# Kernel optimization log

Measured on AMD Instinct MI355X. Metric: run time of the kernel, lower is better.

Reference implementation:

```python
import jax, jax.numpy as jnp
import numpy as np

T, H, DIN, N, E = 2048, 128, 17, 50000, 600000
SMILES_D, KMER_D = 574, 64


def _lstm_bidir(x, w_ih, w_hh, b_ih, b_hh):
    """Bidirectional LSTM layer. x: [T, Din]; weights stacked over direction: [2, 4H, *].
    Torch gate order: i, f, g, o."""
    Hh = w_hh.shape[-1]
    def run(d, reverse):
        xg = x @ w_ih[d].T + b_ih[d] + b_hh[d]  # [T, 4H] precomputed input gates
        def step(carry, xg_t):
            h, c = carry
            g = xg_t + h @ w_hh[d].T
            i, f, gg, o = jnp.split(g, 4)
            c = jax.nn.sigmoid(f) * c + jax.nn.sigmoid(i) * jnp.tanh(gg)
            h = jax.nn.sigmoid(o) * jnp.tanh(c)
            return (h, c), h
        init = (jnp.zeros((Hh,), x.dtype), jnp.zeros((Hh,), x.dtype))
        _, hs = jax.lax.scan(step, init, xg, reverse=reverse)
        return hs
    return jnp.concatenate([run(0, False), run(1, True)], axis=-1)  # [T, 2H]


def _forward(g_mol, feat_seq, smiles, kmer, edge_weight,
             w_ih0, w_hh0, b_ih0, b_hh0, w_ih1, w_hh1, b_ih1, b_hh1,
             Wq, bq, Wk, bk, Wv, bv, Wfc, bfc,
             W_gc1, b_gc1, W_gc2, b_gc2,
             W1, b1, W2, b2, W3, b3, W4, b4,
             edge_src, edge_dst):
    # ---- BiLSTM (2 layers, bidirectional, batch=1) + self-attention ----
    h = _lstm_bidir(g_mol, w_ih0, w_hh0, b_ih0, b_hh0)
    h = _lstm_bidir(h, w_ih1, w_hh1, b_ih1, b_hh1)            # [T, 2H]
    q = h @ Wq.T + bq
    k = h @ Wk.T + bk
    v = h @ Wv.T + bv                                          # [T, H]
    scores = (q @ k.T) / jnp.asarray(H ** 0.5, h.dtype)        # [T, T]
    attn_w = jax.nn.softmax(scores, axis=-1)
    gmol = (attn_w @ v)[-1] @ Wfc.T + bfc                      # [256] (last time step)
    ew = edge_weight[:, None]
    agg1 = jax.ops.segment_sum(feat_seq[edge_src] * ew, edge_dst, num_segments=N)
    h1 = jax.nn.relu(agg1 @ W_gc1 + b_gc1)                     # [N, 128]
    agg2 = jax.ops.segment_sum(h1[edge_src] * ew, edge_dst, num_segments=N)
    h2 = agg2 @ W_gc2 + b_gc2                                  # [N, 256]
    hg = jnp.mean(h2, axis=0)                                  # [256]
    # ---- MLP head ----
    feats = jnp.concatenate([hg, gmol, smiles, kmer])[None, :]  # [1, 1150]
    out = jax.nn.relu(feats @ W1.T + b1)
    out = jax.nn.relu(out @ W2.T + b2)
    out = jax.nn.relu(out @ W3.T + b3)
    out = out @ W4.T + b4                                       # [1, 1]
    return out, attn_w[None]                                    # attn weights [1, T, T]


def setup_inputs() -> dict:
    key = jax.random.key(0)
    ks = jax.random.split(key, 36)
    s = jnp.float32(0.05)
    def rn(k, shape):
        return jax.random.normal(k, shape, jnp.float32) * s
    return {
        "g_mol": jax.random.normal(ks[0], (T, DIN), jnp.float32),
        "feat_seq": jax.random.normal(ks[1], (N, H), jnp.float32),
        "smiles": jax.random.normal(ks[2], (SMILES_D,), jnp.float32),
        "kmer": jax.random.normal(ks[3], (KMER_D,), jnp.float32),
        "edge_weight": jax.random.uniform(ks[4], (E,), jnp.float32),
        "w_ih0": rn(ks[5], (2, 4 * H, DIN)),
        "w_hh0": rn(ks[6], (2, 4 * H, H)),
        "b_ih0": rn(ks[7], (2, 4 * H)),
        "b_hh0": rn(ks[8], (2, 4 * H)),
        "w_ih1": rn(ks[9], (2, 4 * H, 2 * H)),
        "w_hh1": rn(ks[10], (2, 4 * H, H)),
        "b_ih1": rn(ks[11], (2, 4 * H)),
        "b_hh1": rn(ks[12], (2, 4 * H)),
        "Wq": rn(ks[13], (H, 2 * H)), "bq": rn(ks[14], (H,)),
        "Wk": rn(ks[15], (H, 2 * H)), "bk": rn(ks[16], (H,)),
        "Wv": rn(ks[17], (H, 2 * H)), "bv": rn(ks[18], (H,)),
        "Wfc": rn(ks[19], (256, H)), "bfc": rn(ks[20], (256,)),
        "W_gc1": rn(ks[21], (H, H)), "b_gc1": rn(ks[22], (H,)),
        "W_gc2": rn(ks[23], (H, 256)), "b_gc2": rn(ks[24], (256,)),
        "W1": rn(ks[25], (575, 1150)), "b1": rn(ks[26], (575,)),
        "W2": rn(ks[27], (256, 575)), "b2": rn(ks[28], (256,)),
        "W3": rn(ks[29], (64, 256)), "b3": rn(ks[30], (64,)),
        "W4": rn(ks[31], (1, 64)), "b4": rn(ks[32], (1,)),
        "edge_src": jax.random.randint(ks[33], (E,), 0, N),
        "edge_dst": jax.random.randint(ks[34], (E,), 0, N),
    }


def reference(g_mol, feat_seq, smiles, kmer, edge_weight,
              w_ih0, w_hh0, b_ih0, b_hh0, w_ih1, w_hh1, b_ih1, b_hh1,
              Wq, bq, Wk, bk, Wv, bv, Wfc, bfc,
              W_gc1, b_gc1, W_gc2, b_gc2,
              W1, b1, W2, b2, W3, b3, W4, b4,
              edge_src, edge_dst):
    return _forward(g_mol, feat_seq, smiles, kmer, edge_weight,
                    w_ih0, w_hh0, b_ih0, b_hh0, w_ih1, w_hh1, b_ih1, b_hh1,
                    Wq, bq, Wk, bk, Wv, bv, Wfc, bfc,
                    W_gc1, b_gc1, W_gc2, b_gc2,
                    W1, b1, W2, b2, W3, b3, W4, b4,
                    edge_src, edge_dst)
```

## Files before the change

### kernel.cpp

```cpp
#include <hip/hip_runtime.h>
#include <stdint.h>


#define T_SEQ 2048
#define NNODE 50000
#define NEDGE 600000

typedef _Float16 half2_t __attribute__((ext_vector_type(2)));

static __device__ __forceinline__ float fast_rcp(float x) {
#if __has_builtin(__builtin_amdgcn_rcpf)
    return __builtin_amdgcn_rcpf(x);
#else
    return 1.f / x;
#endif
}
static __device__ __forceinline__ float exp2_fast(float x) {
#if __has_builtin(__builtin_amdgcn_exp2f)
    return __builtin_amdgcn_exp2f(x);
#else
    return exp2f(x);
#endif
}

static __device__ __forceinline__ float dot2h(float acc, uint32_t a, uint32_t b) {
#if __has_builtin(__builtin_amdgcn_fdot2)
    return __builtin_amdgcn_fdot2(__builtin_bit_cast(half2_t, a),
                                  __builtin_bit_cast(half2_t, b), acc, false);
#else
    half2_t ha = __builtin_bit_cast(half2_t, a);
    half2_t hb = __builtin_bit_cast(half2_t, b);
    return acc + (float)ha.x * (float)hb.x + (float)ha.y * (float)hb.y;
#endif
}

template<int CTRL>
static __device__ __forceinline__ float qperm(float x) {
    int r = __builtin_amdgcn_update_dpp(0, __builtin_bit_cast(int, x), CTRL, 0xF, 0xF, false);
    return __builtin_bit_cast(float, r);
}
#define QP_XOR1 0xB1
#define QP_XOR2 0x4E
#define QP_XOR3 0x1B

#define SIG_SCALE  (-1.44269504f)
#define TANH_SCALE ( 2.88539008f)

constexpr size_t OFF_XGT   = 0;
constexpr size_t OFF_HT0   = OFF_XGT + 2097152;
constexpr size_t OFF_HT1   = OFF_HT0 + 524288;
constexpr size_t OFF_Q     = OFF_HT1 + 524288;
constexpr size_t OFF_K     = OFF_Q + 262144;
constexpr size_t OFF_V     = OFF_K + 262144;
constexpr size_t OFF_AROW  = OFF_V + 262144;
constexpr size_t OFF_AV    = OFF_AROW + 2048;
constexpr size_t OFF_FEATS = OFF_AV + 128;
constexpr size_t OFF_F1    = OFF_FEATS + 1152;
constexpr size_t OFF_F2    = OFF_F1 + 576;
constexpr size_t OFF_GSUM  = OFF_F2 + 256;
constexpr size_t OFF_OUTW  = OFF_GSUM + 128;
constexpr size_t OFF_DEG   = OFF_OUTW + 50000;
constexpr size_t OFF_ROWP  = OFF_DEG + 50000;
constexpr size_t OFF_CUR   = OFF_ROWP + 50000;
constexpr size_t OFF_WPK   = OFF_CUR + 50000;
constexpr size_t OFF_EPACK = OFF_WPK + 131072;
constexpr size_t WS_WORDS  = OFF_EPACK + 1200000;

__global__ __launch_bounds__(256) void prep_kernel(
    const float* __restrict__ w_hh0, const float* __restrict__ w_hh1,
    uint32_t* __restrict__ wpk)
{
    int i = blockIdx.x * 256 + threadIdx.x;
    if (i >= 131072) return;
    int layer = i >> 16;
    int r = i & 65535;
    int kk = r & 15, m = (r >> 4) & 3, sidx = (r >> 6) & 3, q = (r >> 8) & 127, dirv = (r >> 15) & 1;
    const float* w = layer ? w_hh1 : w_hh0;
    const float* row = w + ((size_t)dirv * 512 + m * 128 + q) * 128;
    int k0 = 32 * sidx + 2 * kk;
    float sc = (m == 2) ? TANH_SCALE : SIG_SCALE;
    half2_t hv;
    hv.x = (_Float16)(row[k0] * sc);
    hv.y = (_Float16)(row[k0 + 1] * sc);
    wpk[i] = __builtin_bit_cast(uint32_t, hv);
}

__global__ __launch_bounds__(512) void xg0_kernel(
    const float* __restrict__ g_mol, const float* __restrict__ w_ih,
    const float* __restrict__ b_ih, const float* __restrict__ b_hh,
    float* __restrict__ xgT)
{
    int b = blockIdx.x;
    int dir = b >> 7, t0 = (b & 127) * 16;
    int r = threadIdx.x;
    __shared__ float xs[272];
    if (r < 272) xs[r] = g_mol[t0 * 17 + r];
    __syncthreads();
    const float* wrow = w_ih + (size_t)(dir * 512 + r) * 17;
    float wv[17];
#pragma unroll
    for (int k = 0; k < 17; ++k) wv[k] = wrow[k];
    float bias = b_ih[dir * 512 + r] + b_hh[dir * 512 + r];
    float rs = ((r >> 7) == 2) ? TANH_SCALE : SIG_SCALE;
    float acc[16];
#pragma unroll
    for (int tt = 0; tt < 16; ++tt) {
        float a = bias;
#pragma unroll
        for (int k = 0; k < 17; ++k) a += xs[tt * 17 + k] * wv[k];
        acc[tt] = a * rs;
    }
    float* orow = xgT + (size_t)(dir * 512 + r) * 2048 + t0;
    *(float4*)(orow + 0)  = make_float4(acc[0], acc[1], acc[2], acc[3]);
    *(float4*)(orow + 4)  = make_float4(acc[4], acc[5], acc[6], acc[7]);
    *(float4*)(orow + 8)  = make_float4(acc[8], acc[9], acc[10], acc[11]);
    *(float4*)(orow + 12) = make_float4(acc[12], acc[13], acc[14], acc[15]);
}

__global__ __launch_bounds__(512) void xg1_kernel(
    const float* __restrict__ hT0, const float* __restrict__ w_ih,
    const float* __restrict__ b_ih, const float* __restrict__ b_hh,
    float* __restrict__ xgT)
{
    int b = blockIdx.x;
    int dir = b >> 7, t0 = (b & 127) * 16;
    int tid = threadIdx.x;
    __shared__ float xs[16 * 256];
    for (int u = tid; u < 1024; u += 512) {
        int k = u >> 2, j4 = u & 3;
        float4 v = *(const float4*)(hT0 + (size_t)k * 2048 + t0 + 4 * j4);
        xs[(4 * j4 + 0) * 256 + k] = v.x;
        xs[(4 * j4 + 1) * 256 + k] = v.y;
        xs[(4 * j4 + 2) * 256 + k] = v.z;
        xs[(4 * j4 + 3) * 256 + k] = v.w;
    }
    __syncthreads();
    int r = tid;
    float bias = b_ih[dir * 512 + r] + b_hh[dir * 512 + r];
    float rs = ((r >> 7) == 2) ? TANH_SCALE : SIG_SCALE;
    float acc[16];
#pragma unroll
    for (int tt = 0; tt < 16; ++tt) acc[tt] = bias;
    const float4* w4 = reinterpret_cast<const float4*>(w_ih + (size_t)(dir * 512 + r) * 256);
    const float4* xs4 = reinterpret_cast<const float4*>(xs);
    for (int k4 = 0; k4 < 64; ++k4) {
        float4 w = w4[k4];
#pragma unroll
        for (int tt = 0; tt < 16; ++tt) {
            float4 x = xs4[tt * 64 + k4];
            acc[tt] += x.x * w.x + x.y * w.y + x.z * w.z + x.w * w.w;
        }
    }
    float* orow = xgT + (size_t)(dir * 512 + r) * 2048 + t0;
    *(float4*)(orow + 0)  = make_float4(acc[0] * rs, acc[1] * rs, acc[2] * rs, acc[3] * rs);
    *(float4*)(orow + 4)  = make_float4(acc[4] * rs, acc[5] * rs, acc[6] * rs, acc[7] * rs);
    *(float4*)(orow + 8)  = make_float4(acc[8] * rs, acc[9] * rs, acc[10] * rs, acc[11] * rs);
    *(float4*)(orow + 12) = make_float4(acc[12] * rs, acc[13] * rs, acc[14] * rs, acc[15] * rs);
}

__global__ __launch_bounds__(512) __attribute__((amdgpu_waves_per_eu(2, 2)))
void lstm_fused_kernel(
    const float* __restrict__ xgT, const uint32_t* __restrict__ wpk,
    float* __restrict__ hT, int mode,
    const int* __restrict__ esrc, const int* __restrict__ edst,
    const float* __restrict__ ew,
    int* __restrict__ deg, float* __restrict__ outw,
    const int* __restrict__ rowp, const uint2* __restrict__ epack,
    const float* __restrict__ feat_seq,
    const float* __restrict__ Wgc1, const float* __restrict__ bgc1,
    float* __restrict__ gsum)
{
    __shared__ __align__(16) float smem[21504];
    const int tid = threadIdx.x;

    if (blockIdx.x >= 2) {
        if (mode == 0) {
            int stride = (gridDim.x - 2) * 512;
            for (int e = (blockIdx.x - 2) * 512 + tid; e < NEDGE; e += stride) {
                atomicAdd(&deg[edst[e]], 1);
                atomicAdd(&outw[esrc[e]], ew[e]);
            }
        } else {
            float* wt   = smem;
            float* bg   = smem + 16384;
            float* aggl = smem + 16512;
            float* gbuf = smem + 17536;
            {
                float4* d4 = (float4*)wt;
                const float4* s4 = (const float4*)Wgc1;
                for (int u = tid; u < 4096; u += 512) d4[u] = s4[u];
                if (tid < 128) { bg[tid] = bgc1[tid]; gbuf[tid] = 0.f; }
            }
            __syncthreads();
            int wv = tid >> 6, lane = tid & 63;
            float ga0 = 0.f, ga1 = 0.f;
            int nwaves = (gridDim.x - 2) * 8;
            for (int n = (blockIdx.x - 2) * 8 + wv; n < NNODE; n += nwaves) {
                int st = rowp[n];
                int dg = deg[n];
                float a0 = 0.f, a1 = 0.f;
                for (int i = 0; i < dg; ++i) {
                    uint2 ep = epack[st + i];
                    float w = __uint_as_float(ep.y);
                    float2 f = *(const float2*)(feat_seq + (size_t)ep.x * 128 + 2 * lane);
                    a0 += w * f.x;
                    a1 += w * f.y;
                }
                *(float2*)&aggl[wv * 128 + 2 * lane] = make_float2(a0, a1);
                float h0 = bg[2 * lane], h1v = bg[2 * lane + 1];
                for (int k = 0; k < 128; ++k) {
                    float av_ = aggl[wv * 128 + k];
                    float2 wv2 = *(const float2*)&wt[k * 128 + 2 * lane];
                    h0 += av_ * wv2.x;
                    h1v += av_ * wv2.y;
                }
                float ow = outw[n];
                ga0 += ow * fmaxf(h0, 0.f);
                ga1 += ow * fmaxf(h1v, 0.f);
            }
            atomicAdd(&gbuf[2 * lane], ga0);
            atomicAdd(&gbuf[2 * lane + 1], ga1);
            __syncthreads();
            if (tid < 128) atomicAdd(&gsum[tid], gbuf[tid]);
        }
        return;
    }

#if __has_builtin(__builtin_amdgcn_s_setprio)
    __builtin_amdgcn_s_setprio(3);
#endif
    const int dir = blockIdx.x;
    const int q = tid >> 2;
    const int s = tid & 3;

    _Float16* hbuf = reinterpret_cast<_Float16*>(smem);

    const uint4* wt4 = reinterpret_cast<const uint4*>(
        wpk + (((size_t)(dir * 128 + q) * 4 + s) * 64));
    uint32_t wr[4][16];
#pragma unroll
    for (int m = 0; m < 4; ++m)
#pragma unroll
        for (int j = 0; j < 4; ++j) {
            uint4 wv = wt4[m * 4 + j];
            wr[m][4 * j + 0] = wv.x; wr[m][4 * j + 1] = wv.y;
            wr[m][4 * j + 2] = wv.z; wr[m][4 * j + 3] = wv.w;
        }

    const float oscale = (s == 2) ? -2.f : 1.f;
    const float obias  = (s == 2) ? 1.f : 0.f;

    if (tid < 128) reinterpret_cast<uint32_t*>(hbuf)[tid] = 0u;
    float c = 0.f;
    float hq[16];
    __syncthreads();

    const float* xrow = xgT + (size_t)(dir * 512 + (s * 128 + q)) * 2048;
    float* hrow = hT + (size_t)(dir * 128 + q) * 2048;

    const int base0 = dir ? 2032 : 0;
    float4 nA = *(const float4*)(xrow + base0);
    float4 nB = *(const float4*)(xrow + base0 + 4);
    float4 nC = *(const float4*)(xrow + base0 + 8);
    float4 nD = *(const float4*)(xrow + base0 + 12);

    for (int s16 = 0; s16 < 128; ++s16) {
        const int base = dir ? (2032 - s16 * 16) : (s16 * 16);
        float4 A = nA, B4 = nB, C4 = nC, D4 = nD;
        if (s16 < 127) {
            const int nb = dir ? (base - 16) : (base + 16);
            nA = *(const float4*)(xrow + nb);
            nB = *(const float4*)(xrow + nb + 4);
            nC = *(const float4*)(xrow + nb + 8);
            nD = *(const float4*)(xrow + nb + 12);
        }
        float xq[16];
        if (dir) {
            xq[0]=D4.w;  xq[1]=D4.z;  xq[2]=D4.y;  xq[3]=D4.x;
            xq[4]=C4.w;  xq[5]=C4.z;  xq[6]=C4.y;  xq[7]=C4.x;
            xq[8]=B4.w;  xq[9]=B4.z;  xq[10]=B4.y; xq[11]=B4.x;
            xq[12]=A.w;  xq[13]=A.z;  xq[14]=A.y;  xq[15]=A.x;
        } else {
            xq[0]=A.x;   xq[1]=A.y;   xq[2]=A.z;   xq[3]=A.w;
            xq[4]=B4.x;  xq[5]=B4.y;  xq[6]=B4.z;  xq[7]=B4.w;
            xq[8]=C4.x;  xq[9]=C4.y;  xq[10]=C4.z; xq[11]=C4.w;
            xq[12]=D4.x; xq[13]=D4.y; xq[14]=D4.z; xq[15]=D4.w;
        }
#pragma unroll
        for (int i = 0; i < 16; ++i) {
            const int p = i & 1;
            const uint4* h4 = reinterpret_cast<const uint4*>(hbuf + p * 128 + s * 32);
            float a0 = 0.f, a1 = 0.f, a2 = 0.f, a3 = 0.f;
#pragma unroll
            for (int j = 0; j < 4; ++j) {
                uint4 hv = h4[j];
                a0 = dot2h(a0, hv.x, wr[0][4 * j + 0]);
                a0 = dot2h(a0, hv.y, wr[0][4 * j + 1]);
                a0 = dot2h(a0, hv.z, wr[0][4 * j + 2]);
                a0 = dot2h(a0, hv.w, wr[0][4 * j + 3]);
                a1 = dot2h(a1, hv.x, wr[1][4 * j + 0]);
                a1 = dot2h(a1, hv.y, wr[1][4 * j + 1]);
                a1 = dot2h(a1, hv.z, wr[1][4 * j + 2]);
                a1 = dot2h(a1, hv.w, wr[1][4 * j + 3]);
                a2 = dot2h(a2, hv.x, wr[2][4 * j + 0]);
                a2 = dot2h(a2, hv.y, wr[2][4 * j + 1]);
                a2 = dot2h(a2, hv.z, wr[2][4 * j + 2]);
                a2 = dot2h(a2, hv.w, wr[2][4 * j + 3]);
                a3 = dot2h(a3, hv.x, wr[3][4 * j + 0]);
                a3 = dot2h(a3, hv.y, wr[3][4 * j + 1]);
                a3 = dot2h(a3, hv.z, wr[3][4 * j + 2]);
                a3 = dot2h(a3, hv.w, wr[3][4 * j + 3]);
            }
            a0 += qperm<QP_XOR1>(a0); a0 += qperm<QP_XOR2>(a0);
            a1 += qperm<QP_XOR1>(a1); a1 += qperm<QP_XOR2>(a1);
            a2 += qperm<QP_XOR1>(a2); a2 += qperm<QP_XOR2>(a2);
            a3 += qperm<QP_XOR1>(a3); a3 += qperm<QP_XOR2>(a3);
            float g01 = (s & 1) ? a1 : a0;
            float g23 = (s & 1) ? a3 : a2;
            float gp = ((s & 2) ? g23 : g01) + xq[i];
            float e = exp2_fast(gp);
            float r = fast_rcp(1.f + e);
            float av_ = fmaf(r, oscale, obias);
            float b1 = qperm<QP_XOR1>(av_);
            float b2 = qperm<QP_XOR2>(av_);
            float b3 = qperm<QP_XOR3>(av_);
            c = fmaf(b1, c, av_ * b2);
            float e2 = exp2_fast(TANH_SCALE * c);
            float r2 = fast_rcp(1.f + e2);
            float hv = b3 * fmaf(-2.f, r2, 1.f);
            if (s == 0) {
                hbuf[(p ^ 1) * 128 + q] = (_Float16)hv;
                hq[dir ? (15 - i) : i] = hv;
            }
            __syncthreads();
        }
        if (s == 0) {
            *(float4*)(hrow + base + 0)  = make_float4(hq[0], hq[1], hq[2], hq[3]);
            *(float4*)(hrow + base + 4)  = make_float4(hq[4], hq[5], hq[6], hq[7]);
            *(float4*)(hrow + base + 8)  = make_float4(hq[8], hq[9], hq[10], hq[11]);
            *(float4*)(hrow + base + 12) = make_float4(hq[12], hq[13], hq[14], hq[15]);
        }
    }
}

__global__ __launch_bounds__(1024) void scan_kernel(
    const int* __restrict__ deg, int* __restrict__ rowp, int* __restrict__ cur)
{
    __shared__ int part[1024];
    int t = threadIdx.x;
    int lo = t * 49, hi = min(lo + 49, NNODE);
    int s = 0;
    for (int i = lo; i < hi; ++i) s += deg[i];
    part[t] = s;
    __syncthreads();
    for (int off = 1; off < 1024; off <<= 1) {
        int v = (t >= off) ? part[t - off] : 0;
        __syncthreads();
        part[t] += v;
        __syncthreads();
    }
    int run = t ? part[t - 1] : 0;
    for (int i = lo; i < hi; ++i) {
        rowp[i] = run;
        cur[i] = run;
        run += deg[i];
    }
}

__global__ __launch_bounds__(512) void fill_kernel(
    const int* __restrict__ esrc, const int* __restrict__ edst,
    const float* __restrict__ ew, int* __restrict__ cur,
    uint2* __restrict__ epack)
{
    int e = blockIdx.x * 512 + threadIdx.x;
    if (e >= NEDGE) return;
    int d = edst[e];
    int pos = atomicAdd(&cur[d], 1);
    epack[pos] = make_uint2((unsigned)esrc[e], __float_as_uint(ew[e]));
}

__global__ __launch_bounds__(384) void qkv_kernel(
    const float* __restrict__ hT1,
    const float* __restrict__ Wq, const float* __restrict__ bq,
    const float* __restrict__ Wk, const float* __restrict__ bk,
    const float* __restrict__ Wv, const float* __restrict__ bv,
    float* __restrict__ q, float* __restrict__ k, float* __restrict__ v)
{
    int t0 = blockIdx.x * 16, tid = threadIdx.x;
    __shared__ float xs[16 * 256];
    for (int u = tid; u < 1024; u += 384) {
        int kk = u >> 2, j4 = u & 3;
        float4 vv = *(const float4*)(hT1 + (size_t)kk * 2048 + t0 + 4 * j4);
        xs[(4 * j4 + 0) * 256 + kk] = vv.x;
        xs[(4 * j4 + 1) * 256 + kk] = vv.y;
        xs[(4 * j4 + 2) * 256 + kk] = vv.z;
        xs[(4 * j4 + 3) * 256 + kk] = vv.w;
    }
    __syncthreads();
    int which = tid >> 7, j = tid & 127;
    const float* W = (which == 0) ? Wq : (which == 1) ? Wk : Wv;
    const float* B = (which == 0) ? bq : (which == 1) ? bk : bv;
    float* out = (which == 0) ? q : (which == 1) ? k : v;
    float bias = B[j];
    float acc[16];
#pragma unroll
    for (int tt = 0; tt < 16; ++tt) acc[tt] = bias;
    const float4* w4 = reinterpret_cast<const float4*>(W + (size_t)j * 256);
    const float4* xs4 = reinterpret_cast<const float4*>(xs);
    for (int k4 = 0; k4 < 64; ++k4) {
        float4 w = w4[k4];
#pragma unroll
        for (int tt = 0; tt < 16; ++tt) {
            float4 x = xs4[tt * 64 + k4];
            acc[tt] += x.x * w.x + x.y * w.y + x.z * w.z + x.w * w.w;
        }
    }
#pragma unroll
    for (int tt = 0; tt < 16; ++tt) out[(size_t)(t0 + tt) * 128 + j] = acc[tt];
}

__global__ __launch_bounds__(256) void scores_kernel(
    const float* __restrict__ q, const float* __restrict__ kmat, float* __restrict__ attn)
{
    int bi = blockIdx.y, bj = blockIdx.x, tid = threadIdx.x;
    __shared__ float qs[16][132];
    __shared__ float ks[16][132];
    for (int u = tid; u < 2048; u += 256) {
        int rr = u >> 7, cc = u & 127;
        qs[rr][cc] = q[(size_t)(bi * 16 + rr) * 128 + cc];
        ks[rr][cc] = kmat[(size_t)(bj * 16 + rr) * 128 + cc];
    }
    __syncthreads();
    int ty = tid >> 4, tx = tid & 15;
    const float4* qrow = reinterpret_cast<const float4*>(&qs[ty][0]);
    const float4* krow = reinterpret_cast<const float4*>(&ks[tx][0]);
    float acc = 0.f;
#pragma unroll
    for (int c4 = 0; c4 < 32; ++c4) {
        float4 a = qrow[c4], b = krow[c4];
        acc += a.x * b.x + a.y * b.y + a.z * b.z + a.w * b.w;
    }
    attn[(size_t)(bi * 16 + ty) * 2048 + (bj * 16 + tx)] = acc * 0.08838834764831845f;
}

__global__ __launch_bounds__(256) void softmax_kernel(
    float* __restrict__ attn, float* __restrict__ attnrow)
{
    int i = blockIdx.x, tid = threadIdx.x;
    float* row = attn + (size_t)i * 2048;
    __shared__ float red[256];
    float m = -1e30f;
    for (int j = tid; j < 2048; j += 256) m = fmaxf(m, row[j]);
    red[tid] = m; __syncthreads();
    for (int s = 128; s > 0; s >>= 1) { if (tid < s) red[tid] = fmaxf(red[tid], red[tid + s]); __syncthreads(); }
    m = red[0]; __syncthreads();
    float sum = 0.f;
    for (int j = tid; j < 2048; j += 256) sum += __expf(row[j] - m);
    red[tid] = sum; __syncthreads();
    for (int s = 128; s > 0; s >>= 1) { if (tid < s) red[tid] += red[tid + s]; __syncthreads(); }
    float inv = 1.f / red[0];
    for (int j = tid; j < 2048; j += 256) {
        float w = __expf(row[j] - m) * inv;
        row[j] = w;
        if (i == 2047) attnrow[j] = w;
    }
}

__global__ __launch_bounds__(128) void av_kernel(
    const float* __restrict__ attnrow, const float* __restrict__ v, float* __restrict__ av)
{
    int j = threadIdx.x;
    float acc = 0.f;
#pragma unroll 8
    for (int t = 0; t < 2048; ++t) acc += attnrow[t] * v[(size_t)t * 128 + j];
    av[j] = acc;
}

__global__ __launch_bounds__(256) void gmolfc_kernel(
    const float* __restrict__ av, const float* __restrict__ Wfc, const float* __restrict__ bfc,
    float* __restrict__ feats)
{
    int o = threadIdx.x;
    __shared__ float a[128];
    if (o < 128) a[o] = av[o];
    __syncthreads();
    const float4* w4 = reinterpret_cast<const float4*>(Wfc + (size_t)o * 128);
    const float4* a4 = reinterpret_cast<const float4*>(a);
    float acc = bfc[o];
#pragma unroll 8
    for (int kk = 0; kk < 32; ++kk) {
        float4 w = w4[kk], x = a4[kk];
        acc += x.x * w.x + x.y * w.y + x.z * w.z + x.w * w.w;
    }
    feats[256 + o] = acc;
}

__global__ __launch_bounds__(256) void feats_kernel(
    const float* __restrict__ gsum, const float* __restrict__ W_gc2, const float* __restrict__ b_gc2,
    const float* __restrict__ smiles, const float* __restrict__ kmer, float* __restrict__ feats)
{
    int i = blockIdx.x * 256 + threadIdx.x;
    if (i < 256) {
        float dotv = 0.f;
#pragma unroll 4
        for (int k = 0; k < 128; ++k) dotv += gsum[k] * W_gc2[(size_t)k * 256 + i];
        feats[i] = b_gc2[i] + dotv * (1.f / (float)NNODE);
    } else if (i >= 512 && i < 1086) {
        feats[i] = smiles[i - 512];
    } else if (i >= 1086 && i < 1150) {
        feats[i] = kmer[i - 1086];
    }
}

__global__ __launch_bounds__(256) void mlp1_kernel(
    const float* __restrict__ feats, const float* __restrict__ W1, const float* __restrict__ b1,
    float* __restrict__ f1)
{
    int o = blockIdx.x, tid = threadIdx.x;
    const float* w = W1 + (size_t)o * 1150;
    float acc = 0.f;
    for (int k = tid; k < 1150; k += 256) acc += feats[k] * w[k];
    __shared__ float red[256];
    red[tid] = acc; __syncthreads();
    for (int s = 128; s > 0; s >>= 1) { if (tid < s) red[tid] += red[tid + s]; __syncthreads(); }
    if (tid == 0) f1[o] = fmaxf(red[0] + b1[o], 0.f);
}

__global__ __launch_bounds__(256) void mlp2_kernel(
    const float* __restrict__ f1, const float* __restrict__ W2, const float* __restrict__ b2,
    float* __restrict__ f2)
{
    int o = blockIdx.x, tid = threadIdx.x;
    const float* w = W2 + (size_t)o * 575;
    float acc = 0.f;
    for (int k = tid; k < 575; k += 256) acc += f1[k] * w[k];
    __shared__ float red[256];
    red[tid] = acc; __syncthreads();
    for (int s = 128; s > 0; s >>= 1) { if (tid < s) red[tid] += red[tid + s]; __syncthreads(); }
    if (tid == 0) f2[o] = fmaxf(red[0] + b2[o], 0.f);
}

__global__ __launch_bounds__(256) void mlp_tail_kernel(
    const float* __restrict__ f2,
    const float* __restrict__ W3, const float* __restrict__ b3,
    const float* __restrict__ W4, const float* __restrict__ b4,
    float* __restrict__ out)
{
    __shared__ float f2s[256];
    __shared__ float f3[64];
    int tid = threadIdx.x;
    f2s[tid] = f2[tid];
    __syncthreads();
    if (tid < 64) {
        const float* w = W3 + (size_t)tid * 256;
        float acc = b3[tid];
        for (int k = 0; k < 256; ++k) acc += f2s[k] * w[k];
        f3[tid] = fmaxf(acc, 0.f);
    }
    __syncthreads();
    if (tid == 0) {
        float acc = b4[0];
        for (int k = 0; k < 64; ++k) acc += f3[k] * W4[k];
        out[0] = acc;
    }
}

extern "C" void kernel_launch(void* const* d_in, const int* in_sizes, int n_in,
                              void* d_out, int out_size, void* d_ws, size_t ws_size,
                              hipStream_t stream)
{
    const float* g_mol   = (const float*)d_in[0];
    const float* feat_seq= (const float*)d_in[1];
    const float* smiles  = (const float*)d_in[2];
    const float* kmer    = (const float*)d_in[3];
    const float* edge_w  = (const float*)d_in[4];
    const float* w_ih0   = (const float*)d_in[5];
    const float* w_hh0   = (const float*)d_in[6];
    const float* b_ih0   = (const float*)d_in[7];
    const float* b_hh0   = (const float*)d_in[8];
    const float* w_ih1   = (const float*)d_in[9];
    const float* w_hh1   = (const float*)d_in[10];
    const float* b_ih1   = (const float*)d_in[11];
    const float* b_hh1   = (const float*)d_in[12];
    const float* Wq      = (const float*)d_in[13];
    const float* bq      = (const float*)d_in[14];
    const float* Wk      = (const float*)d_in[15];
    const float* bk      = (const float*)d_in[16];
    const float* Wv      = (const float*)d_in[17];
    const float* bv      = (const float*)d_in[18];
    const float* Wfc     = (const float*)d_in[19];
    const float* bfc     = (const float*)d_in[20];
    const float* W_gc1   = (const float*)d_in[21];
    const float* b_gc1   = (const float*)d_in[22];
    const float* W_gc2   = (const float*)d_in[23];
    const float* b_gc2   = (const float*)d_in[24];
    const float* W1      = (const float*)d_in[25];
    const float* b1      = (const float*)d_in[26];
    const float* W2      = (const float*)d_in[27];
    const float* b2      = (const float*)d_in[28];
    const float* W3      = (const float*)d_in[29];
    const float* b3      = (const float*)d_in[30];
    const float* W4      = (const float*)d_in[31];
    const float* b4      = (const float*)d_in[32];
    const int* esrc      = (const int*)d_in[33];
    const int* edst      = (const int*)d_in[34];

    float* ws    = (float*)d_ws;
    float* xgT   = ws + OFF_XGT;
    float* hT0   = ws + OFF_HT0;
    float* hT1   = ws + OFF_HT1;
    float* q     = ws + OFF_Q;
    float* k     = ws + OFF_K;
    float* v     = ws + OFF_V;
    float* arow  = ws + OFF_AROW;
    float* av    = ws + OFF_AV;
    float* feats = ws + OFF_FEATS;
    float* f1    = ws + OFF_F1;
    float* f2    = ws + OFF_F2;
    float* gsum  = ws + OFF_GSUM;
    float* outw  = ws + OFF_OUTW;
    int*   deg   = (int*)(ws + OFF_DEG);
    int*   rowp  = (int*)(ws + OFF_ROWP);
    int*   cur   = (int*)(ws + OFF_CUR);
    uint32_t* wpk = (uint32_t*)(ws + OFF_WPK);
    uint2* epack = (uint2*)(ws + OFF_EPACK);

    float* out_f = (float*)d_out;
    float* attn  = out_f + 1;

    hipMemsetAsync(gsum, 0, (size_t)(128 + 50000 + 50000) * sizeof(float), stream);

    prep_kernel<<<512, 256, 0, stream>>>(w_hh0, w_hh1, wpk);
    xg0_kernel<<<256, 512, 0, stream>>>(g_mol, w_ih0, b_ih0, b_hh0, xgT);

    lstm_fused_kernel<<<256, 512, 0, stream>>>(
        xgT, wpk, hT0, 0, esrc, edst, edge_w, deg, outw,
        rowp, epack, feat_seq, W_gc1, b_gc1, gsum);

    scan_kernel<<<1, 1024, 0, stream>>>(deg, rowp, cur);
    fill_kernel<<<1172, 512, 0, stream>>>(esrc, edst, edge_w, cur, epack);

    xg1_kernel<<<256, 512, 0, stream>>>(hT0, w_ih1, b_ih1, b_hh1, xgT);
    lstm_fused_kernel<<<256, 512, 0, stream>>>(
        xgT, wpk + 65536, hT1, 1, esrc, edst, edge_w, deg, outw,
        rowp, epack, feat_seq, W_gc1, b_gc1, gsum);

    qkv_kernel<<<128, 384, 0, stream>>>(hT1, Wq, bq, Wk, bk, Wv, bv, q, k, v);
    scores_kernel<<<dim3(128, 128), 256, 0, stream>>>(q, k, attn);
    softmax_kernel<<<2048, 256, 0, stream>>>(attn, arow);
    av_kernel<<<1, 128, 0, stream>>>(arow, v, av);
    gmolfc_kernel<<<1, 256, 0, stream>>>(av, Wfc, bfc, feats);
    feats_kernel<<<5, 256, 0, stream>>>(gsum, W_gc2, b_gc2, smiles, kmer, feats);

    mlp1_kernel<<<575, 256, 0, stream>>>(feats, W1, b1, f1);
    mlp2_kernel<<<256, 256, 0, stream>>>(f1, W2, b2, f2);
    mlp_tail_kernel<<<1, 256, 0, stream>>>(f2, W3, b3, W4, b4, out_f);
}
```

Measured before the change: 2.531 ms.

## Compute LSTM recurrent matvec with MFMA 16x16x32 f16 instead of fdot2

The recurrent h·W_hh product in the LSTM scan moves from per-thread fdot2 chains with DPP reductions to MFMA 16x16x32 f16 instructions. The weights are repacked into MFMA B-fragment layout and held in registers. Blocks shrink to 256 threads with one wave per EU, and each lane now computes all four gates for its hidden unit, which removes the cross-lane gate shuffles. The per-step x-gate loads become scalar prefetches, and hT is stored per step instead of in 16-step batches. The MFMA computes a full 16-row tile of which only one row is useful, so most of that work is wasted. The graph-side blocks sharing this kernel also lose half their threads.

After: 4.006 ms. +58.3%, slower.

```diff
diff --git a/kernel.cpp b/kernel.cpp
--- a/kernel.cpp
+++ b/kernel.cpp
@@ -6,7 +6,8 @@
 #define NNODE 50000
 #define NEDGE 600000
 
-typedef _Float16 half2_t __attribute__((ext_vector_type(2)));
+typedef _Float16 half8 __attribute__((ext_vector_type(8)));
+typedef float float4v __attribute__((ext_vector_type(4)));
 
 static __device__ __forceinline__ float fast_rcp(float x) {
 #if __has_builtin(__builtin_amdgcn_rcpf)
@@ -22,26 +23,6 @@
     return exp2f(x);
 #endif
 }
-
-static __device__ __forceinline__ float dot2h(float acc, uint32_t a, uint32_t b) {
-#if __has_builtin(__builtin_amdgcn_fdot2)
-    return __builtin_amdgcn_fdot2(__builtin_bit_cast(half2_t, a),
-                                  __builtin_bit_cast(half2_t, b), acc, false);
-#else
-    half2_t ha = __builtin_bit_cast(half2_t, a);
-    half2_t hb = __builtin_bit_cast(half2_t, b);
-    return acc + (float)ha.x * (float)hb.x + (float)ha.y * (float)hb.y;
-#endif
-}
-
-template<int CTRL>
-static __device__ __forceinline__ float qperm(float x) {
-    int r = __builtin_amdgcn_update_dpp(0, __builtin_bit_cast(int, x), CTRL, 0xF, 0xF, false);
-    return __builtin_bit_cast(float, r);
-}
-#define QP_XOR1 0xB1
-#define QP_XOR2 0x4E
-#define QP_XOR3 0x1B
 
 #define SIG_SCALE  (-1.44269504f)
 #define TANH_SCALE ( 2.88539008f)
@@ -72,17 +53,24 @@
 {
     int i = blockIdx.x * 256 + threadIdx.x;
     if (i >= 131072) return;
+    int jp = i & 3;
+    int L  = (i >> 2) & 63;
+    int kc = (i >> 8) & 3;
+    int t  = (i >> 10) & 7;
+    int w  = (i >> 13) & 3;
+    int d  = (i >> 15) & 1;
     int layer = i >> 16;
-    int r = i & 65535;
-    int kk = r & 15, m = (r >> 4) & 3, sidx = (r >> 6) & 3, q = (r >> 8) & 127, dirv = (r >> 15) & 1;
-    const float* w = layer ? w_hh1 : w_hh0;
-    const float* row = w + ((size_t)dirv * 512 + m * 128 + q) * 128;
-    int k0 = 32 * sidx + 2 * kk;
+    int m = t & 3, cg = t >> 2;
+    const float* W = layer ? w_hh1 : w_hh0;
+    int row = d * 512 + m * 128 + 32 * w + 16 * cg + (L & 15);
+    int col = kc * 32 + (L >> 4) * 8 + 2 * jp;
     float sc = (m == 2) ? TANH_SCALE : SIG_SCALE;
-    half2_t hv;
-    hv.x = (_Float16)(row[k0] * sc);
-    hv.y = (_Float16)(row[k0 + 1] * sc);
-    wpk[i] = __builtin_bit_cast(uint32_t, hv);
+    _Float16 h2[2];
+    h2[0] = (_Float16)(W[(size_t)row * 128 + col] * sc);
+    h2[1] = (_Float16)(W[(size_t)row * 128 + col + 1] * sc);
+    uint32_t u;
+    __builtin_memcpy(&u, h2, 4);
+    wpk[i] = u;
 }
 
 __global__ __launch_bounds__(512) void xg0_kernel(
@@ -158,7 +146,7 @@
     *(float4*)(orow + 12) = make_float4(acc[12] * rs, acc[13] * rs, acc[14] * rs, acc[15] * rs);
 }
 
-__global__ __launch_bounds__(512) __attribute__((amdgpu_waves_per_eu(2, 2)))
+__global__ __launch_bounds__(256) __attribute__((amdgpu_waves_per_eu(1, 1)))
 void lstm_fused_kernel(
     const float* __restrict__ xgT, const uint32_t* __restrict__ wpk,
     float* __restrict__ hT, int mode,
@@ -175,8 +163,8 @@
 
     if (blockIdx.x >= 2) {
         if (mode == 0) {
-            int stride = (gridDim.x - 2) * 512;
-            for (int e = (blockIdx.x - 2) * 512 + tid; e < NEDGE; e += stride) {
+            int stride = (gridDim.x - 2) * 256;
+            for (int e = (blockIdx.x - 2) * 256 + tid; e < NEDGE; e += stride) {
                 atomicAdd(&deg[edst[e]], 1);
                 atomicAdd(&outw[esrc[e]], ew[e]);
             }
@@ -188,14 +176,14 @@
             {
                 float4* d4 = (float4*)wt;
                 const float4* s4 = (const float4*)Wgc1;
-                for (int u = tid; u < 4096; u += 512) d4[u] = s4[u];
+                for (int u = tid; u < 4096; u += 256) d4[u] = s4[u];
                 if (tid < 128) { bg[tid] = bgc1[tid]; gbuf[tid] = 0.f; }
             }
             __syncthreads();
             int wv = tid >> 6, lane = tid & 63;
             float ga0 = 0.f, ga1 = 0.f;
-            int nwaves = (gridDim.x - 2) * 8;
-            for (int n = (blockIdx.x - 2) * 8 + wv; n < NNODE; n += nwaves) {
+            int nwaves = (gridDim.x - 2) * 4;
+            for (int n = (blockIdx.x - 2) * 4 + wv; n < NNODE; n += nwaves) {
                 int st = rowp[n];
                 int dg = deg[n];
                 float a0 = 0.f, a1 = 0.f;
@@ -230,116 +218,82 @@
     __builtin_amdgcn_s_setprio(3);
 #endif
     const int dir = blockIdx.x;
-    const int q = tid >> 2;
-    const int s = tid & 3;
+    const int w   = tid >> 6;
+    const int L   = tid & 63;
+    const int rg  = L >> 4;
+    const bool hi = (rg & 1);
+    const int o0  = 32 * w + (L & 15);
+    const int osel = hi ? (o0 + 16) : o0;
 
     _Float16* hbuf = reinterpret_cast<_Float16*>(smem);
 
-    const uint4* wt4 = reinterpret_cast<const uint4*>(
-        wpk + (((size_t)(dir * 128 + q) * 4 + s) * 64));
-    uint32_t wr[4][16];
-#pragma unroll
-    for (int m = 0; m < 4; ++m)
-#pragma unroll
-        for (int j = 0; j < 4; ++j) {
-            uint4 wv = wt4[m * 4 + j];
-            wr[m][4 * j + 0] = wv.x; wr[m][4 * j + 1] = wv.y;
-            wr[m][4 * j + 2] = wv.z; wr[m][4 * j + 3] = wv.w;
-        }
-
-    const float oscale = (s == 2) ? -2.f : 1.f;
-    const float obias  = (s == 2) ? 1.f : 0.f;
+    const half8* wsrc = reinterpret_cast<const half8*>(wpk) + ((size_t)(dir * 4 + w) * 32) * 64;
+    half8 bw[8][4];
+#pragma unroll
+    for (int t = 0; t < 8; ++t)
+#pragma unroll
+        for (int kc = 0; kc < 4; ++kc)
+            bw[t][kc] = wsrc[(t * 4 + kc) * 64 + L];
 
     if (tid < 128) reinterpret_cast<uint32_t*>(hbuf)[tid] = 0u;
     float c = 0.f;
-    float hq[16];
-    __syncthreads();
-
-    const float* xrow = xgT + (size_t)(dir * 512 + (s * 128 + q)) * 2048;
-    float* hrow = hT + (size_t)(dir * 128 + q) * 2048;
-
-    const int base0 = dir ? 2032 : 0;
-    float4 nA = *(const float4*)(xrow + base0);
-    float4 nB = *(const float4*)(xrow + base0 + 4);
-    float4 nC = *(const float4*)(xrow + base0 + 8);
-    float4 nD = *(const float4*)(xrow + base0 + 12);
-
-    for (int s16 = 0; s16 < 128; ++s16) {
-        const int base = dir ? (2032 - s16 * 16) : (s16 * 16);
-        float4 A = nA, B4 = nB, C4 = nC, D4 = nD;
-        if (s16 < 127) {
-            const int nb = dir ? (base - 16) : (base + 16);
-            nA = *(const float4*)(xrow + nb);
-            nB = *(const float4*)(xrow + nb + 4);
-            nC = *(const float4*)(xrow + nb + 8);
-            nD = *(const float4*)(xrow + nb + 12);
-        }
-        float xq[16];
-        if (dir) {
-            xq[0]=D4.w;  xq[1]=D4.z;  xq[2]=D4.y;  xq[3]=D4.x;
-            xq[4]=C4.w;  xq[5]=C4.z;  xq[6]=C4.y;  xq[7]=C4.x;
-            xq[8]=B4.w;  xq[9]=B4.z;  xq[10]=B4.y; xq[11]=B4.x;
-            xq[12]=A.w;  xq[13]=A.z;  xq[14]=A.y;  xq[15]=A.x;
-        } else {
-            xq[0]=A.x;   xq[1]=A.y;   xq[2]=A.z;   xq[3]=A.w;
-            xq[4]=B4.x;  xq[5]=B4.y;  xq[6]=B4.z;  xq[7]=B4.w;
-            xq[8]=C4.x;  xq[9]=C4.y;  xq[10]=C4.z; xq[11]=C4.w;
-            xq[12]=D4.x; xq[13]=D4.y; xq[14]=D4.z; xq[15]=D4.w;
-        }
-#pragma unroll
-        for (int i = 0; i < 16; ++i) {
-            const int p = i & 1;
-            const uint4* h4 = reinterpret_cast<const uint4*>(hbuf + p * 128 + s * 32);
-            float a0 = 0.f, a1 = 0.f, a2 = 0.f, a3 = 0.f;
-#pragma unroll
-            for (int j = 0; j < 4; ++j) {
-                uint4 hv = h4[j];
-                a0 = dot2h(a0, hv.x, wr[0][4 * j + 0]);
-                a0 = dot2h(a0, hv.y, wr[0][4 * j + 1]);
-                a0 = dot2h(a0, hv.z, wr[0][4 * j + 2]);
-                a0 = dot2h(a0, hv.w, wr[0][4 * j + 3]);
-                a1 = dot2h(a1, hv.x, wr[1][4 * j + 0]);
-                a1 = dot2h(a1, hv.y, wr[1][4 * j + 1]);
-                a1 = dot2h(a1, hv.z, wr[1][4 * j + 2]);
-                a1 = dot2h(a1, hv.w, wr[1][4 * j + 3]);
-                a2 = dot2h(a2, hv.x, wr[2][4 * j + 0]);
-                a2 = dot2h(a2, hv.y, wr[2][4 * j + 1]);
-                a2 = dot2h(a2, hv.z, wr[2][4 * j + 2]);
-                a2 = dot2h(a2, hv.w, wr[2][4 * j + 3]);
-                a3 = dot2h(a3, hv.x, wr[3][4 * j + 0]);
-                a3 = dot2h(a3, hv.y, wr[3][4 * j + 1]);
-                a3 = dot2h(a3, hv.z, wr[3][4 * j + 2]);
-                a3 = dot2h(a3, hv.w, wr[3][4 * j + 3]);
-            }
-            a0 += qperm<QP_XOR1>(a0); a0 += qperm<QP_XOR2>(a0);
-            a1 += qperm<QP_XOR1>(a1); a1 += qperm<QP_XOR2>(a1);
-            a2 += qperm<QP_XOR1>(a2); a2 += qperm<QP_XOR2>(a2);
-            a3 += qperm<QP_XOR1>(a3); a3 += qperm<QP_XOR2>(a3);
-            float g01 = (s & 1) ? a1 : a0;
-            float g23 = (s & 1) ? a3 : a2;
-            float gp = ((s & 2) ? g23 : g01) + xq[i];
-            float e = exp2_fast(gp);
-            float r = fast_rcp(1.f + e);
-            float av_ = fmaf(r, oscale, obias);
-            float b1 = qperm<QP_XOR1>(av_);
-            float b2 = qperm<QP_XOR2>(av_);
-            float b3 = qperm<QP_XOR3>(av_);
-            c = fmaf(b1, c, av_ * b2);
-            float e2 = exp2_fast(TANH_SCALE * c);
-            float r2 = fast_rcp(1.f + e2);
-            float hv = b3 * fmaf(-2.f, r2, 1.f);
-            if (s == 0) {
-                hbuf[(p ^ 1) * 128 + q] = (_Float16)hv;
-                hq[dir ? (15 - i) : i] = hv;
-            }
-            __syncthreads();
-        }
-        if (s == 0) {
-            *(float4*)(hrow + base + 0)  = make_float4(hq[0], hq[1], hq[2], hq[3]);
-            *(float4*)(hrow + base + 4)  = make_float4(hq[4], hq[5], hq[6], hq[7]);
-            *(float4*)(hrow + base + 8)  = make_float4(hq[8], hq[9], hq[10], hq[11]);
-            *(float4*)(hrow + base + 12) = make_float4(hq[12], hq[13], hq[14], hq[15]);
-        }
+    __syncthreads();
+
+    const float* xgb = xgT + (size_t)(dir * 512 + osel) * 2048;
+    float* hrow = hT + (size_t)(dir * 128 + osel) * 2048;
+    const bool dost = (L < 32);
+
+    const int tt0 = dir ? 2047 : 0;
+    float xc0 = xgb[tt0];
+    float xc1 = xgb[tt0 + 262144];
+    float xc2 = xgb[tt0 + 524288];
+    float xc3 = xgb[tt0 + 786432];
+
+    const float4v zro = {0.f, 0.f, 0.f, 0.f};
+
+    for (int i = 0; i < 2048; ++i) {
+        const int p = i & 1;
+        const int tt = dir ? (2047 - i) : i;
+        const int inx = (i + 1 < 2048) ? (i + 1) : i;
+        const int tn = dir ? (2047 - inx) : inx;
+
+        const char* hbase = reinterpret_cast<const char*>(hbuf) + p * 256 + rg * 16;
+        half8 Af[4];
+#pragma unroll
+        for (int kc = 0; kc < 4; ++kc)
+            Af[kc] = *reinterpret_cast<const half8*>(hbase + kc * 64);
+
+        float4v ac[8];
+#pragma unroll
+        for (int t = 0; t < 8; ++t)
+            ac[t] = __builtin_amdgcn_mfma_f32_16x16x32_f16(Af[0], bw[t][0], zro, 0, 0, 0);
+#pragma unroll
+        for (int kc = 1; kc < 4; ++kc)
+#pragma unroll
+            for (int t = 0; t < 8; ++t)
+                ac[t] = __builtin_amdgcn_mfma_f32_16x16x32_f16(Af[kc], bw[t][kc], ac[t], 0, 0, 0);
+
+        float xn0 = xgb[tn];
+        float xn1 = xgb[tn + 262144];
+        float xn2 = xgb[tn + 524288];
+        float xn3 = xgb[tn + 786432];
+
+        float g0 = (hi ? ac[4].x : ac[0].x) + xc0;
+        float g1 = (hi ? ac[5].x : ac[1].x) + xc1;
+        float g2 = (hi ? ac[6].x : ac[2].x) + xc2;
+        float g3 = (hi ? ac[7].x : ac[3].x) + xc3;
+        float iv = fast_rcp(1.f + exp2_fast(g0));
+        float fv = fast_rcp(1.f + exp2_fast(g1));
+        float gv = fmaf(-2.f, fast_rcp(1.f + exp2_fast(g2)), 1.f);
+        float ov = fast_rcp(1.f + exp2_fast(g3));
+        c = fmaf(fv, c, iv * gv);
+        float th = fmaf(-2.f, fast_rcp(1.f + exp2_fast(TANH_SCALE * c)), 1.f);
+        float hv = ov * th;
+
+        hbuf[(p ^ 1) * 128 + osel] = (_Float16)hv;
+        if (dost) hrow[tt] = hv;
+        __syncthreads();
+        xc0 = xn0; xc1 = xn1; xc2 = xn2; xc3 = xn3;
     }
 }
 
@@ -633,7 +587,7 @@
     prep_kernel<<<512, 256, 0, stream>>>(w_hh0, w_hh1, wpk);
     xg0_kernel<<<256, 512, 0, stream>>>(g_mol, w_ih0, b_ih0, b_hh0, xgT);
 
-    lstm_fused_kernel<<<256, 512, 0, stream>>>(
+    lstm_fused_kernel<<<256, 256, 0, stream>>>(
         xgT, wpk, hT0, 0, esrc, edst, edge_w, deg, outw,
         rowp, epack, feat_seq, W_gc1, b_gc1, gsum);
 
@@ -641,7 +595,7 @@
     fill_kernel<<<1172, 512, 0, stream>>>(esrc, edst, edge_w, cur, epack);
 
     xg1_kernel<<<256, 512, 0, stream>>>(hT0, w_ih1, b_ih1, b_hh1, xgT);
-    lstm_fused_kernel<<<256, 512, 0, stream>>>(
+    lstm_fused_kernel<<<256, 256, 0, stream>>>(
         xgT, wpk + 65536, hT1, 1, esrc, edst, edge_w, deg, outw,
         rowp, epack, feat_seq, W_gc1, b_gc1, gsum);
 
```
